# Optimization experiments

Measured on AMD Instinct MI355X. Metric: run time of the kernel, lower is better.

Reference implementation:

```python
import jax, jax.numpy as jnp
import numpy as np

B = 1
T_FRAMES = 512
LDIM = 512
D = 512
H = 8
DH = 64
L = 8
FF = 2048
CTX = 250
RATIOS = (8, 6, 5, 4)
MAX_PERIOD = 10000.0


def setup_inputs() -> dict:
    key = jax.random.key(0)
    ks = iter(jax.random.split(key, 80))
    def rn(shape, s=0.02):
        return jax.random.normal(next(ks), shape, jnp.float32) * s
    inp = {}
    inp['latent'] = rn((B, LDIM, T_FRAMES), 1.0)
    inp['emb_std'] = jax.random.uniform(next(ks), (LDIM,), jnp.float32, 0.5, 1.5)
    inp['emb_mean'] = rn((LDIM,), 0.1)
    inp['quant_w'] = rn((D, LDIM)); inp['quant_b'] = jnp.zeros((D,))
    inp['up_w'] = rn((D, D, 4)); inp['up_b'] = jnp.zeros((D,))
    inp['n1w'] = jnp.ones((L, D)); inp['n1b'] = jnp.zeros((L, D))
    inp['ipw'] = rn((L, 3 * D, D)); inp['ipb'] = jnp.zeros((L, 3 * D))
    inp['opw'] = rn((L, D, D)); inp['opb'] = jnp.zeros((L, D))
    inp['ls1'] = jnp.full((L, D), 0.01)
    inp['n2w'] = jnp.ones((L, D)); inp['n2b'] = jnp.zeros((L, D))
    inp['l1w'] = rn((L, FF, D)); inp['l1b'] = jnp.zeros((L, FF))
    inp['l2w'] = rn((L, D, FF)); inp['l2b'] = jnp.zeros((L, D))
    inp['ls2'] = jnp.full((L, D), 0.01)
    inp['tproj_w'] = rn((D, D)); inp['tproj_b'] = jnp.zeros((D,))
    inp['dc0_w'] = rn((1024, D, 7)); inp['dc0_b'] = jnp.zeros((1024,))
    ch = 1024
    for i, r in enumerate(RATIOS, 1):
        co = ch // 2
        inp['t%d_w' % i] = rn((ch, co, 2 * r)); inp['t%d_b' % i] = jnp.zeros((co,))
        inp['r%da_w' % i] = rn((co // 2, co, 3)); inp['r%da_b' % i] = jnp.zeros((co // 2,))
        inp['r%db_w' % i] = rn((co, co // 2, 1)); inp['r%db_b' % i] = jnp.zeros((co,))
        ch = co
    inp['df_w'] = rn((1, 64, 7)); inp['df_b'] = jnp.zeros((1,))
    return {k: jnp.asarray(v, jnp.float32) for k, v in inp.items()}


def _ln(x, w, b):
    m = x.mean(-1, keepdims=True)
    v = ((x - m) ** 2).mean(-1, keepdims=True)
    return (x - m) / jnp.sqrt(v + 1e-5) * w + b


def _rope(x, cos, sin):
    # x: (B,T,H,DH); cos/sin: (T,1,DH//2)
    b_, t_, h_, d_ = x.shape
    xr = x.reshape(b_, t_, h_, d_ // 2, 2)
    re, im = xr[..., 0], xr[..., 1]
    out = jnp.stack([re * cos - im * sin, re * sin + im * cos], axis=-1)
    return out.reshape(b_, t_, h_, d_)


def _conv(x, w, b, stride=1):
    # StreamingConv1d non-streaming: left-pad by k-stride (zeros), then valid conv.
    k = w.shape[-1]
    pad = k - stride
    if pad > 0:
        x = jnp.pad(x, ((0, 0), (0, 0), (pad, 0)))
    y = jax.lax.conv_general_dilated(x, w, (stride,), 'VALID',
                                     dimension_numbers=('NCH', 'OIH', 'NCH'))
    return y + b[None, :, None]


def _convtr(x, w, b, stride):
    # torch ConvTranspose1d, padding=0: w is (in, out, k); L_out=(L-1)*stride+k
    k = w.shape[-1]
    w2 = jnp.swapaxes(jnp.flip(w, -1), 0, 1)  # (out, in, k)
    y = jax.lax.conv_general_dilated(x, w2, (1,), [(k - 1, k - 1)],
                                     lhs_dilation=(stride,),
                                     dimension_numbers=('NCH', 'OIH', 'NCH'))
    return y + b[None, :, None]


def _forward(latent, emb_std, emb_mean, quant_w, quant_b, up_w, up_b,
             n1w, n1b, ipw, ipb, opw, opb, ls1, n2w, n2b, l1w, l1b, l2w, l2b, ls2,
             tproj_w, tproj_b, dc0_w, dc0_b,
             t1_w, t1_b, r1a_w, r1a_b, r1b_w, r1b_b,
             t2_w, t2_b, r2a_w, r2a_b, r2b_w, r2b_b,
             t3_w, t3_b, r3a_w, r3a_b, r3b_w, r3b_b,
             t4_w, t4_b, r4a_w, r4a_b, r4b_w, r4b_b,
             df_w, df_b):
    # denormalize + quantizer output proj (1x1 conv)
    x = latent * emb_std[None, :, None] + emb_mean[None, :, None]
    x = jnp.einsum('od,bdt->bot', quant_w, x) + quant_b[None, :, None]
    # upsample (raw convtr, no trimming)
    x = _convtr(x, up_w, up_b, 2)
    z = jnp.swapaxes(x, 1, 2)  # (B, T, D)
    T = z.shape[1]
    # windowed causal additive mask: attend to previous `CTX` positions incl. self
    pos = jnp.arange(T)
    delta = pos[:, None] - pos[None, :]
    mask = jnp.where((delta >= 0) & (delta < CTX), 0.0, -jnp.inf).astype(jnp.float32)
    # RoPE tables (offset = 0)
    fr = jnp.exp(jnp.arange(DH // 2, dtype=jnp.float32) * (-np.log(MAX_PERIOD) * 2.0 / DH))
    ang = jnp.arange(T, dtype=jnp.float32)[:, None, None] * fr  # (T,1,DH//2)
    cos, sin = jnp.cos(ang), jnp.sin(ang)
    scale = 1.0 / np.sqrt(DH)

    def step(h, p):
        n1w_, n1b_, ipw_, ipb_, opw_, opb_, ls1_, n2w_, n2b_, l1w_, l1b_, l2w_, l2b_, ls2_ = p
        hn = _ln(h, n1w_, n1b_)
        qkv = (jnp.einsum('btd,ed->bte', hn, ipw_) + ipb_).reshape(B, T, 3, H, DH)
        q, k, v = qkv[:, :, 0], qkv[:, :, 1], qkv[:, :, 2]
        q = _rope(q, cos, sin)
        k = _rope(k, cos, sin)
        s = jnp.einsum('bqhd,bkhd->bhqk', q, k) * scale + mask
        a = jax.nn.softmax(s, axis=-1)
        o = jnp.einsum('bhqk,bkhd->bqhd', a, v).reshape(B, T, D)
        o = jnp.einsum('btd,ed->bte', o, opw_) + opb_
        h = h + ls1_ * o
        hn2 = _ln(h, n2w_, n2b_)
        ff = jax.nn.gelu(jnp.einsum('btd,fd->btf', hn2, l1w_) + l1b_, approximate=False)
        ff = jnp.einsum('btf,df->btd', ff, l2w_) + l2b_
        h = h + ls2_ * ff
        return h, None

    z, _ = jax.lax.scan(step, z, (n1w, n1b, ipw, ipb, opw, opb, ls1,
                                  n2w, n2b, l1w, l1b, l2w, l2b, ls2))
    z = jnp.einsum('btd,ed->bte', z, tproj_w) + tproj_b
    z = jnp.swapaxes(z, 1, 2)  # (B, D, T)
    # SEANet decoder
    z = _conv(z, dc0_w, dc0_b, 1)
    stages = ((t1_w, t1_b, r1a_w, r1a_b, r1b_w, r1b_b, 8),
              (t2_w, t2_b, r2a_w, r2a_b, r2b_w, r2b_b, 6),
              (t3_w, t3_b, r3a_w, r3a_b, r3b_w, r3b_b, 5),
              (t4_w, t4_b, r4a_w, r4a_b, r4b_w, r4b_b, 4))
    for tw, tb, raw_, rab_, rbw_, rbb_, st in stages:
        z = jax.nn.elu(z)
        z = _convtr(z, tw, tb, st)
        v2 = _conv(jax.nn.elu(z), raw_, rab_, 1)
        v2 = _conv(jax.nn.elu(v2), rbw_, rbb_, 1)
        z = z + v2  # residual block skip
    z = jax.nn.elu(z)
    z = _conv(z, df_w, df_b, 1)
    return z  # (B, 1, T_samples)


def reference(latent, emb_std, emb_mean, quant_w, quant_b, up_w, up_b,
              n1w, n1b, ipw, ipb, opw, opb, ls1, n2w, n2b, l1w, l1b, l2w, l2b, ls2,
              tproj_w, tproj_b, dc0_w, dc0_b,
              t1_w, t1_b, r1a_w, r1a_b, r1b_w, r1b_b,
              t2_w, t2_b, r2a_w, r2a_b, r2b_w, r2b_b,
              t3_w, t3_b, r3a_w, r3a_b, r3b_w, r3b_b,
              t4_w, t4_b, r4a_w, r4a_b, r4b_w, r4b_b,
              df_w, df_b):
    return _forward(latent, emb_std, emb_mean, quant_w, quant_b, up_w, up_b,
                    n1w, n1b, ipw, ipb, opw, opb, ls1, n2w, n2b, l1w, l1b, l2w, l2b, ls2,
                    tproj_w, tproj_b, dc0_w, dc0_b,
                    t1_w, t1_b, r1a_w, r1a_b, r1b_w, r1b_b,
                    t2_w, t2_b, r2a_w, r2a_b, r2b_w, r2b_b,
                    t3_w, t3_b, r3a_w, r3a_b, r3b_w, r3b_b,
                    t4_w, t4_b, r4a_w, r4a_b, r4b_w, r4b_b,
                    df_w, df_b)
```

## Files before the change

### kernel.cpp

```cpp
#include <hip/hip_runtime.h>
#include <math.h>

typedef __attribute__((ext_vector_type(8))) short short8;
typedef __attribute__((ext_vector_type(4))) float f32x4;

#define MFMA16(a, b, c) __builtin_amdgcn_mfma_f32_16x16x32_bf16((a), (b), (c), 0, 0, 0)

__device__ __forceinline__ unsigned bfu(float f) {
    unsigned u = __float_as_uint(f);
    return (u + 0x7fffu + ((u >> 16) & 1u)) >> 16;
}

__device__ __forceinline__ void swz_block(unsigned& bx, unsigned& by, unsigned& bz) {
    unsigned gx = gridDim.x, gy = gridDim.y, gz = gridDim.z;
    unsigned nb = gx * gy * gz;
    unsigned d = blockIdx.x + gx * (blockIdx.y + gy * blockIdx.z);
    if ((nb & 7u) == 0u) d = (d & 7u) * (nb >> 3) + (d >> 3);
    bx = d % gx;
    unsigned r = d / gx;
    by = r % gy;
    bz = r / gy;
}

static constexpr int TT   = 1026;
static constexpr int T_S1 = 8216;
static constexpr int T_S2 = 49302;
static constexpr int T_S3 = 246515;
static constexpr int T_S4 = 986064;

static constexpr int NCH    = 8;
static constexpr int LC     = T_S4 / NCH;
static constexpr int LE_MAX = LC + 8;

static constexpr size_t O_X0  = 0;
static constexpr size_t O_XQ  = 262144;
static constexpr size_t O_XU  = 524288;
static constexpr size_t O_Z   = 1049600;
static constexpr size_t O_HN  = 1574912;
static constexpr size_t O_QKV = 2100224;
static constexpr size_t O_AO  = 3676160;
static constexpr size_t O_FF  = 4201472;
static constexpr size_t O_COS = 6302720;
static constexpr size_t O_SIN = 6335552;
static constexpr size_t O_ZT  = 6368384;
static constexpr size_t O_ZC  = 6893696;
static constexpr size_t O_D0  = 7419008;
static constexpr size_t O_Z1  = 8469632;
static constexpr size_t O_V1  = 12676224;
static constexpr size_t O_PS1 = 16000000;
static constexpr size_t O_Z2  = 31553920;
static constexpr size_t O_V2  = 0;
static constexpr size_t O_Z3  = 0;
static constexpr size_t O_V3  = 31553920;
static constexpr size_t O_Z4C = 31553920;
static constexpr size_t O_VAC = 39442944;
static constexpr size_t O_WS4 = 43388928;
static constexpr size_t O_WS3 = 44176256;

static inline int cdiv(int a, int b) { return (a + b - 1) / b; }

__global__ __launch_bounds__(256) void addp_k(float* __restrict__ y,
    const float* __restrict__ p, unsigned long long pstr, int np, int n4)
{
    int i = blockIdx.x * 256 + threadIdx.x;
    if (i >= n4) return;
    float4 s = ((float4*)y)[i];
    for (int z = 0; z < np; z++) {
        float4 q = ((const float4*)(p + (size_t)z * pstr))[i];
        s.x += q.x; s.y += q.y; s.z += q.z; s.w += q.w;
    }
    ((float4*)y)[i] = s;
}

__global__ __launch_bounds__(256) void wreorder_tr(const float* __restrict__ w,
    float* __restrict__ wp, int Ci, int Co, int S, int n)
{
    int i = blockIdx.x * 256 + threadIdx.x;
    if (i >= n) return;
    int o = i / (Ci * 2), r = i - o * (Ci * 2);
    int ci = r >> 1, j = r & 1;
    int co = o / S, p = o - co * S;
    wp[i] = w[((size_t)ci * Co + co) * (2 * S) + (1 - j) * S + p];
}

__global__ __launch_bounds__(256) void embed_k(const float* __restrict__ lat,
    const float* __restrict__ sd, const float* __restrict__ mn, float* __restrict__ y)
{
    int i = blockIdx.x * 256 + threadIdx.x;
    if (i >= 512 * 512) return;
    int c = i >> 9;
    y[i] = lat[i] * sd[c] + mn[c];
}

__global__ __launch_bounds__(256) void rope_tables(float* __restrict__ cs, float* __restrict__ sn)
{
    int idx = blockIdx.x * 256 + threadIdx.x;
    if (idx >= TT * 32) return;
    int i = idx & 31;
    int t = idx >> 5;
    float fr = expf(-(float)i * (logf(10000.f) / 32.f));
    float ang = (float)t * fr;
    cs[idx] = cosf(ang);
    sn[idx] = sinf(ang);
}

__global__ __launch_bounds__(256) void rope_apply(float* __restrict__ qkv,
    const float* __restrict__ cs, const float* __restrict__ sn)
{
    int idx = blockIdx.x * 256 + threadIdx.x;
    if (idx >= TT * 8 * 32) return;
    int i = idx & 31;
    int h = (idx >> 5) & 7;
    int t = idx >> 8;
    float c = cs[t * 32 + i], s = sn[t * 32 + i];
    size_t base = (size_t)t * 1536 + h * 64 + 2 * i;
    float re = qkv[base], im = qkv[base + 1];
    qkv[base]     = re * c - im * s;
    qkv[base + 1] = re * s + im * c;
    base += 512;
    re = qkv[base]; im = qkv[base + 1];
    qkv[base]     = re * c - im * s;
    qkv[base + 1] = re * s + im * c;
}

__global__ __launch_bounds__(256) void transpose_k(const float* __restrict__ in,
    float* __restrict__ out, int R, int C)
{
    __shared__ float tile[32][33];
    int c0 = blockIdx.x * 32, r0 = blockIdx.y * 32;
    int tx = threadIdx.x & 31, ty = threadIdx.x >> 5;
    for (int dy = ty; dy < 32; dy += 8) {
        int r = r0 + dy, c = c0 + tx;
        tile[dy][tx] = (r < R && c < C) ? in[(size_t)r * C + c] : 0.f;
    }
    __syncthreads();
    for (int dy = ty; dy < 32; dy += 8) {
        int c = c0 + dy, r = r0 + tx;
        if (c < C && r < R) out[(size_t)c * R + r] = tile[tx][dy];
    }
}

__global__ __launch_bounds__(256) void ln_kernel(const float* __restrict__ x,
    const float* __restrict__ w, const float* __restrict__ b, float* __restrict__ y)
{
    int t = blockIdx.x, tid = threadIdx.x;
    const float* xr = x + (size_t)t * 512;
    float v0 = xr[tid], v1 = xr[tid + 256];
    float s = v0 + v1, q = v0 * v0 + v1 * v1;
    for (int off = 32; off; off >>= 1) {
        s += __shfl_down(s, off);
        q += __shfl_down(q, off);
    }
    __shared__ float ss[4], qq[4], mb[2];
    int wid = tid >> 6, lane = tid & 63;
    if (lane == 0) { ss[wid] = s; qq[wid] = q; }
    __syncthreads();
    if (tid == 0) {
        float S = ss[0] + ss[1] + ss[2] + ss[3];
        float Q = qq[0] + qq[1] + qq[2] + qq[3];
        float m = S * (1.f / 512.f);
        float var = Q * (1.f / 512.f) - m * m;
        mb[0] = m;
        mb[1] = rsqrtf(var + 1e-5f);
    }
    __syncthreads();
    float m = mb[0], inv = mb[1];
    y[(size_t)t * 512 + tid]       = (v0 - m) * inv * w[tid] + b[tid];
    y[(size_t)t * 512 + tid + 256] = (v1 - m) * inv * w[tid + 256] + b[tid + 256];
}

__global__ __launch_bounds__(256) void attn_kernel(const float* __restrict__ qkv,
    float* __restrict__ o)
{
    int t = blockIdx.x, h = blockIdx.y, tid = threadIdx.x;
    __shared__ float sq[64];
    __shared__ float sp[256];
    __shared__ float red[256];
    __shared__ float pacc[4][64];
    int klo = t - 249; if (klo < 0) klo = 0;
    int kc = t - klo + 1;
    if (tid < 64) sq[tid] = qkv[(size_t)t * 1536 + h * 64 + tid];
    __syncthreads();
    float sval = -3.0e38f;
    if (tid < kc) {
        const float* kr = qkv + (size_t)(klo + tid) * 1536 + 512 + h * 64;
        float d = 0.f;
#pragma unroll 8
        for (int i = 0; i < 64; i++) d += sq[i] * kr[i];
        sval = d * 0.125f;
    }
    red[tid] = sval;
    __syncthreads();
    for (int s2 = 128; s2 > 0; s2 >>= 1) {
        if (tid < s2) red[tid] = fmaxf(red[tid], red[tid + s2]);
        __syncthreads();
    }
    float m = red[0];
    __syncthreads();
    float p = (tid < kc) ? __expf(sval - m) : 0.f;
    sp[tid] = p;
    red[tid] = p;
    __syncthreads();
    for (int s2 = 128; s2 > 0; s2 >>= 1) {
        if (tid < s2) red[tid] += red[tid + s2];
        __syncthreads();
    }
    float inv = 1.f / red[0];
    int d = tid & 63, g = tid >> 6;
    float a = 0.f;
#pragma unroll 4
    for (int kk = g; kk < kc; kk += 4)
        a += sp[kk] * qkv[(size_t)(klo + kk) * 1536 + 1024 + h * 64 + d];
    pacc[g][d] = a;
    __syncthreads();
    if (tid < 64) {
        float r = (pacc[0][tid] + pacc[1][tid] + pacc[2][tid] + pacc[3][tid]) * inv;
        o[(size_t)t * 512 + h * 64 + tid] = r;
    }
}

template <int EPI>
__global__ __launch_bounds__(256, 3) void mfma_gemm(const float* __restrict__ A,
    const float* __restrict__ Wt, const float* __restrict__ bias,
    const float* __restrict__ ls, float* __restrict__ C, int M, int N, int K)
{
    constexpr int STR = 72;
    __shared__ unsigned short sA[128 * STR];
    __shared__ unsigned short sB[128 * STR];
    int tid = threadIdx.x;
    unsigned bxs, bys, bzs; swz_block(bxs, bys, bzs);
    int m0 = bys * 128, n0 = bxs * 128;
    int w = tid >> 6, lane = tid & 63;
    int wm = (w >> 1) * 64, wn = (w & 1) * 64;
    int row15 = lane & 15, q8 = (lane >> 4) * 8;
    int rb = tid >> 3;
    int sg = (tid & 7) * 8;
    f32x4 acc[4][4] = {};
    float4 av[8], bv[8];
    const float4 z4 = make_float4(0.f, 0.f, 0.f, 0.f);

    auto prefetch = [&](int k0) {
#pragma unroll
        for (int it = 0; it < 4; it++) {
            int r = rb + it * 32;
            int gm = m0 + r;
            if (gm < M) {
                const float4* p = (const float4*)(A + (size_t)gm * K + k0 + sg);
                av[2 * it] = p[0]; av[2 * it + 1] = p[1];
            } else { av[2 * it] = z4; av[2 * it + 1] = z4; }
            int gn = n0 + r;
            if (gn < N) {
                const float4* p = (const float4*)(Wt + (size_t)gn * K + k0 + sg);
                bv[2 * it] = p[0]; bv[2 * it + 1] = p[1];
            } else { bv[2 * it] = z4; bv[2 * it + 1] = z4; }
        }
    };

    prefetch(0);
    for (int k0 = 0; k0 < K; k0 += 64) {
        __syncthreads();
#pragma unroll
        for (int it = 0; it < 4; it++) {
            int r = rb + it * 32;
            unsigned* d = (unsigned*)&sA[r * STR + sg];
            float4 f0 = av[2 * it], f1 = av[2 * it + 1];
            d[0] = bfu(f0.x) | (bfu(f0.y) << 16); d[1] = bfu(f0.z) | (bfu(f0.w) << 16);
            d[2] = bfu(f1.x) | (bfu(f1.y) << 16); d[3] = bfu(f1.z) | (bfu(f1.w) << 16);
            d = (unsigned*)&sB[r * STR + sg];
            f0 = bv[2 * it]; f1 = bv[2 * it + 1];
            d[0] = bfu(f0.x) | (bfu(f0.y) << 16); d[1] = bfu(f0.z) | (bfu(f0.w) << 16);
            d[2] = bfu(f1.x) | (bfu(f1.y) << 16); d[3] = bfu(f1.z) | (bfu(f1.w) << 16);
        }
        __syncthreads();
        if (k0 + 64 < K) prefetch(k0 + 64);
#pragma unroll
        for (int kk = 0; kk < 64; kk += 32) {
            short8 af[4], bf[4];
#pragma unroll
            for (int f = 0; f < 4; f++) {
                af[f] = *(const short8*)&sA[(wm + f * 16 + row15) * STR + kk + q8];
                bf[f] = *(const short8*)&sB[(wn + f * 16 + row15) * STR + kk + q8];
            }
#pragma unroll
            for (int i = 0; i < 4; i++)
#pragma unroll
                for (int j = 0; j < 4; j++)
                    acc[i][j] = MFMA16(af[i], bf[j], acc[i][j]);
        }
    }
    int rq = (lane >> 4) * 4;
#pragma unroll
    for (int i = 0; i < 4; i++) {
#pragma unroll
        for (int r = 0; r < 4; r++) {
            int m = m0 + wm + i * 16 + rq + r;
            if (m >= M) continue;
#pragma unroll
            for (int j = 0; j < 4; j++) {
                int n = n0 + wn + j * 16 + row15;
                float v = acc[i][j][r] + bias[n];
                size_t idx = (size_t)m * N + n;
                if (EPI == 0) C[idx] = v;
                else if (EPI == 1) C[idx] = 0.5f * v * (1.f + erff(v * 0.70710678118654752f));
                else C[idx] += ls[n] * v;
            }
        }
    }
}

template <int K, int SHF, bool ELU_IN, bool ACC, bool PART>
__global__ __launch_bounds__(256, 2) void mfma_conv(
    const float* __restrict__ x, const float* __restrict__ w,
    const float* __restrict__ bias, float* __restrict__ y, float* __restrict__ part,
    unsigned long long pstr,
    int Ci, int Co, int x_str, int Tx, int x_t0, int Ty, int y_t0, int to_lo, int to_hi,
    int sh_lo, int sh_hi, int nz)
{
    constexpr int TL = 128 + K - 1;
    constexpr int SX = 40;
    constexpr int SW = 40;
    constexpr int NX = (32 * TL + 255) / 256;
    constexpr int NW4 = 2 * K;
    constexpr int LTS = (SHF > 0) ? 64 * 130 : 1;
    __shared__ unsigned short sX[TL * SX];
    __shared__ unsigned short sW[K * 64 * SW];
    __shared__ float ldsT[LTS];
    int tid = threadIdx.x;
    unsigned bxs, bys, bzs; swz_block(bxs, bys, bzs);
    int co0 = bys * 64;
    int t_base = to_lo + bxs * 128;
    int zi = (int)bzs;
    int cpz = (Ci / 32) / nz;
    int ci_b = zi * cpz * 32, ci_e = ci_b + cpz * 32;
    int w_id = tid >> 6, lane = tid & 63;
    int wm = (w_id >> 1) * 32, wn = (w_id & 1) * 64;
    int row15 = lane & 15, q8 = (lane >> 4) * 8;
    f32x4 acc[2][4] = {};
    float xv[NX];
    float4 wv4[NW4];
    const float4 z4 = make_float4(0.f, 0.f, 0.f, 0.f);

    auto prefetch = [&](int ci0) {
#pragma unroll
        for (int it = 0; it < NX; it++) {
            int i = tid + it * 256;
            float v = 0.f;
            if (i < 32 * TL) {
                int ci = i / TL, tl = i - ci * TL;
                int gl = t_base - (K - 1) + tl - x_t0;
                if (gl >= 0 && gl < Tx) v = x[(size_t)(ci0 + ci) * x_str + gl];
            }
            xv[it] = v;
        }
#pragma unroll
        for (int it = 0; it < NW4; it++) {
            int i4 = tid + it * 256;
            int co = i4 / (8 * K), r4 = i4 - co * (8 * K);
            wv4[it] = (co0 + co < Co)
                ? *(const float4*)(w + ((size_t)(co0 + co) * Ci + ci0) * K + r4 * 4)
                : z4;
        }
    };
    auto commit = [&]() {
#pragma unroll
        for (int it = 0; it < NX; it++) {
            int i = tid + it * 256;
            if (i < 32 * TL) {
                int ci = i / TL, tl = i - ci * TL;
                float v = xv[it];
                if (ELU_IN) v = v > 0.f ? v : __expf(v) - 1.f;
                sX[tl * SX + ci] = (unsigned short)bfu(v);
            }
        }
#pragma unroll
        for (int it = 0; it < NW4; it++) {
            int i4 = tid + it * 256;
            int co = i4 / (8 * K), r4 = i4 - co * (8 * K);
            float4 f = wv4[it];
#pragma unroll
            for (int e = 0; e < 4; e++) {
                int k = r4 * 4 + e;
                int ci = k / K, j = k - ci * K;
                float fv = (e == 0) ? f.x : (e == 1) ? f.y : (e == 2) ? f.z : f.w;
                sW[(j * 64 + co) * SW + ci] = (unsigned short)bfu(fv);
            }
        }
    };

    prefetch(ci_b);
    for (int ci0 = ci_b; ci0 < ci_e; ci0 += 32) {
        __syncthreads();
        commit();
        __syncthreads();
        if (ci0 + 32 < ci_e) prefetch(ci0 + 32);
#pragma unroll
        for (int j = 0; j < K; j++) {
            short8 af[2], bf[4];
#pragma unroll
            for (int f = 0; f < 2; f++)
                af[f] = *(const short8*)&sW[(j * 64 + wm + f * 16 + row15) * SW + q8];
#pragma unroll
            for (int f = 0; f < 4; f++)
                bf[f] = *(const short8*)&sX[(wn + f * 16 + row15 + j) * SX + q8];
#pragma unroll
            for (int i = 0; i < 2; i++)
#pragma unroll
                for (int f = 0; f < 4; f++)
                    acc[i][f] = MFMA16(af[i], bf[f], acc[i][f]);
        }
    }
    int rq = (lane >> 4) * 4;
    if constexpr (SHF > 0) {
        __syncthreads();
#pragma unroll
        for (int i = 0; i < 2; i++) {
#pragma unroll
            for (int r = 0; r < 4; r++) {
                int ol = wm + i * 16 + rq + r;
                float b = bias[(co0 + ol) / SHF];
#pragma unroll
                for (int f = 0; f < 4; f++) {
                    int tl = wn + f * 16 + row15;
                    ldsT[ol * 130 + tl] = acc[i][f][r] + b;
                }
            }
        }
        __syncthreads();
        int co_lo = co0 / SHF;
        int cnt = (co0 + 63) / SHF - co_lo + 1;
        int tot = cnt * 128 * SHF;
        for (int e = tid; e < tot; e += 256) {
            int cr = e / (128 * SHF), u = e - cr * (128 * SHF);
            int t_rel = u / SHF, p = u - t_rel * SHF;
            int co = co_lo + cr;
            int o = co * SHF + p - co0;
            int to = (t_base + t_rel) * SHF + p;
            if (o >= 0 && o < 64 && to >= sh_lo && to < sh_hi)
                y[(size_t)co * Ty + (to - y_t0)] = ldsT[o * 130 + t_rel];
        }
    } else {
#pragma unroll
        for (int i = 0; i < 2; i++) {
#pragma unroll
            for (int r = 0; r < 4; r++) {
                int co = co0 + wm + i * 16 + rq + r;
                if (co >= Co) continue;
                float b = bias[co];
#pragma unroll
                for (int f = 0; f < 4; f++) {
                    int t = t_base + wn + f * 16 + row15;
                    if (t < to_hi) {
                        size_t idx = (size_t)co * Ty + (t - y_t0);
                        if (PART && zi > 0) {
                            part[(size_t)(zi - 1) * pstr + idx] = acc[i][f][r];
                        } else {
                            float v = acc[i][f][r] + b;
                            if (ACC) y[idx] += v; else y[idx] = v;
                        }
                    }
                }
            }
        }
    }
}

__global__ __launch_bounds__(256) void conv7_out_chunk(const float* __restrict__ z4c,
    const float* __restrict__ w, const float* __restrict__ bias,
    float* __restrict__ out, int ext0, int t0, int cnt)
{
    __shared__ float ws_w[64 * 7];
    int tl = blockIdx.x * 256 + threadIdx.x;
    for (int i = threadIdx.x; i < 448; i += 256) ws_w[i] = w[i];
    __syncthreads();
    if (tl >= cnt) return;
    int t = t0 + tl;
    float acc = bias[0];
    for (int ci = 0; ci < 64; ci++) {
        const float* xr = z4c + (size_t)ci * LE_MAX;
#pragma unroll
        for (int j = 0; j < 7; j++) {
            int tg = t - 6 + j;
            float v = 0.f;
            if (tg >= 0) {
                float z = xr[tg - ext0];
                v = z > 0.f ? z : __expf(z) - 1.f;
            }
            acc += ws_w[ci * 7 + j] * v;
        }
    }
    out[t] = acc;
}

template <int K, bool ELU_IN, bool ACC, bool PART>
static void conv_launch(const float* x, const float* w, const float* b, float* y,
    float* part, unsigned long long pstr,
    int Ci, int Co, int x_str, int Tx, int x_t0, int Ty, int y_t0, int to_lo, int to_hi,
    int nz, hipStream_t stream)
{
    dim3 g(cdiv(to_hi - to_lo, 128), cdiv(Co, 64), nz);
    mfma_conv<K, 0, ELU_IN, ACC, PART><<<g, 256, 0, stream>>>(x, w, b, y, part, pstr,
        Ci, Co, x_str, Tx, x_t0, Ty, y_t0, to_lo, to_hi, 0, 0, nz);
}

template <int S, bool ELU_IN>
static void convtr2_launch(const float* x, const float* wp, const float* b, float* y,
    int Ci, int Co, int Ti, int Ty, int y_t0, int to_lo, int to_hi, hipStream_t stream)
{
    int q_lo = to_lo / S;
    int q_hi = cdiv(to_hi, S);
    dim3 g(cdiv(q_hi - q_lo, 128), (Co * S) / 64, 1);
    mfma_conv<2, S, ELU_IN, false, false><<<g, 256, 0, stream>>>(x, wp, b, y, nullptr, 0,
        Ci, Co * S, Ti, Ti, 0, Ty, y_t0, q_lo, q_hi, to_lo, to_hi, 1);
}

extern "C" void kernel_launch(void* const* d_in, const int* in_sizes, int n_in,
                              void* d_out, int out_size, void* d_ws, size_t ws_size,
                              hipStream_t stream)
{
    const float* latent  = (const float*)d_in[0];
    const float* emb_std = (const float*)d_in[1];
    const float* emb_mean= (const float*)d_in[2];
    const float* quant_w = (const float*)d_in[3];
    const float* quant_b = (const float*)d_in[4];
    const float* up_w    = (const float*)d_in[5];
    const float* up_b    = (const float*)d_in[6];
    const float* n1w     = (const float*)d_in[7];
    const float* n1b     = (const float*)d_in[8];
    const float* ipw     = (const float*)d_in[9];
    const float* ipb     = (const float*)d_in[10];
    const float* opw     = (const float*)d_in[11];
    const float* opb     = (const float*)d_in[12];
    const float* ls1     = (const float*)d_in[13];
    const float* n2w     = (const float*)d_in[14];
    const float* n2b     = (const float*)d_in[15];
    const float* l1w     = (const float*)d_in[16];
    const float* l1b     = (const float*)d_in[17];
    const float* l2w     = (const float*)d_in[18];
    const float* l2b     = (const float*)d_in[19];
    const float* ls2     = (const float*)d_in[20];
    const float* tproj_w = (const float*)d_in[21];
    const float* tproj_b = (const float*)d_in[22];
    const float* dc0_w   = (const float*)d_in[23];
    const float* dc0_b   = (const float*)d_in[24];
    const float* df_w    = (const float*)d_in[49];
    const float* df_b    = (const float*)d_in[50];

    float* W = (float*)d_ws;
    float* OUT = (float*)d_out;

    embed_k<<<cdiv(512 * 512, 256), 256, 0, stream>>>(latent, emb_std, emb_mean, W + O_X0);
    conv_launch<1, false, false, true>(W + O_X0, quant_w, quant_b, W + O_XQ,
        W + O_QKV, 262144ULL, 512, 512, 512, 512, 0, 512, 0, 0, 512, 4, stream);
    addp_k<<<cdiv(262144 / 4, 256), 256, 0, stream>>>(W + O_XQ, W + O_QKV, 262144ULL, 3, 262144 / 4);
    wreorder_tr<<<cdiv(1048576, 256), 256, 0, stream>>>(up_w, W + O_QKV, 512, 512, 2, 1048576);
    convtr2_launch<2, false>(W + O_XQ, W + O_QKV, up_b, W + O_XU,
        512, 512, 512, TT, 0, 0, TT, stream);
    transpose_k<<<dim3(cdiv(TT, 32), cdiv(512, 32)), 256, 0, stream>>>(W + O_XU, W + O_Z, 512, TT);
    rope_tables<<<cdiv(TT * 32, 256), 256, 0, stream>>>(W + O_COS, W + O_SIN);

    for (int l = 0; l < 8; l++) {
        ln_kernel<<<TT, 256, 0, stream>>>(W + O_Z, n1w + l * 512, n1b + l * 512, W + O_HN);
        mfma_gemm<0><<<dim3(1536 / 128, cdiv(TT, 128)), 256, 0, stream>>>(
            W + O_HN, ipw + (size_t)l * 1536 * 512, ipb + l * 1536, nullptr, W + O_QKV, TT, 1536, 512);
        rope_apply<<<cdiv(TT * 8 * 32, 256), 256, 0, stream>>>(W + O_QKV, W + O_COS, W + O_SIN);
        attn_kernel<<<dim3(TT, 8), 256, 0, stream>>>(W + O_QKV, W + O_AO);
        mfma_gemm<2><<<dim3(512 / 128, cdiv(TT, 128)), 256, 0, stream>>>(
            W + O_AO, opw + (size_t)l * 512 * 512, opb + l * 512, ls1 + l * 512, W + O_Z, TT, 512, 512);
        ln_kernel<<<TT, 256, 0, stream>>>(W + O_Z, n2w + l * 512, n2b + l * 512, W + O_HN);
        mfma_gemm<1><<<dim3(2048 / 128, cdiv(TT, 128)), 256, 0, stream>>>(
            W + O_HN, l1w + (size_t)l * 2048 * 512, l1b + l * 2048, nullptr, W + O_FF, TT, 2048, 512);
        mfma_gemm<2><<<dim3(512 / 128, cdiv(TT, 128)), 256, 0, stream>>>(
            W + O_FF, l2w + (size_t)l * 512 * 2048, l2b + l * 512, ls2 + l * 512, W + O_Z, TT, 512, 2048);
    }

    mfma_gemm<0><<<dim3(512 / 128, cdiv(TT, 128)), 256, 0, stream>>>(
        W + O_Z, tproj_w, tproj_b, nullptr, W + O_ZT, TT, 512, 512);
    transpose_k<<<dim3(cdiv(512, 32), cdiv(TT, 32)), 256, 0, stream>>>(W + O_ZT, W + O_ZC, TT, 512);
    conv_launch<7, false, false, true>(W + O_ZC, dc0_w, dc0_b, W + O_D0,
        W + O_FF, 1050624ULL, 512, 1024, TT, TT, 0, TT, 0, 0, TT, 2, stream);
    addp_k<<<cdiv(1050624 / 4, 256), 256, 0, stream>>>(W + O_D0, W + O_FF, 1050624ULL, 1, 1050624 / 4);

    {
        const float* tw = (const float*)d_in[25]; const float* tb = (const float*)d_in[26];
        const float* raw = (const float*)d_in[27]; const float* rab = (const float*)d_in[28];
        const float* rbw = (const float*)d_in[29]; const float* rbb = (const float*)d_in[30];
        wreorder_tr<<<cdiv(8388608, 256), 256, 0, stream>>>(tw, W + O_PS1, 1024, 512, 8, 8388608);
        convtr2_launch<8, true>(W + O_D0, W + O_PS1, tb, W + O_Z1,
            1024, 512, TT, T_S1, 0, 0, T_S1, stream);
        conv_launch<3, true, false, true>(W + O_Z1, raw, rab, W + O_V1,
            W + O_PS1, 2103296ULL, 512, 256, T_S1, T_S1, 0, T_S1, 0, 0, T_S1, 2, stream);
        addp_k<<<cdiv(2103296 / 4, 256), 256, 0, stream>>>(W + O_V1, W + O_PS1, 2103296ULL, 1, 2103296 / 4);
        conv_launch<1, true, true, false>(W + O_V1, rbw, rbb, W + O_Z1,
            nullptr, 0ULL, 256, 512, T_S1, T_S1, 0, T_S1, 0, 0, T_S1, 1, stream);
    }
    {
        const float* tw = (const float*)d_in[31]; const float* tb = (const float*)d_in[32];
        const float* raw = (const float*)d_in[33]; const float* rab = (const float*)d_in[34];
        const float* rbw = (const float*)d_in[35]; const float* rbb = (const float*)d_in[36];
        wreorder_tr<<<cdiv(1572864, 256), 256, 0, stream>>>(tw, W + O_PS1, 512, 256, 6, 1572864);
        convtr2_launch<6, true>(W + O_Z1, W + O_PS1, tb, W + O_Z2,
            512, 256, T_S1, T_S2, 0, 0, T_S2, stream);
        conv_launch<3, true, false, false>(W + O_Z2, raw, rab, W + O_V2,
            nullptr, 0ULL, 256, 128, T_S2, T_S2, 0, T_S2, 0, 0, T_S2, 1, stream);
        conv_launch<1, true, true, false>(W + O_V2, rbw, rbb, W + O_Z2,
            nullptr, 0ULL, 128, 256, T_S2, T_S2, 0, T_S2, 0, 0, T_S2, 1, stream);
    }
    {
        const float* tw = (const float*)d_in[37]; const float* tb = (const float*)d_in[38];
        const float* raw = (const float*)d_in[39]; const float* rab = (const float*)d_in[40];
        const float* rbw = (const float*)d_in[41]; const float* rbb = (const float*)d_in[42];
        wreorder_tr<<<cdiv(327680, 256), 256, 0, stream>>>(tw, W + O_WS3, 256, 128, 5, 327680);
        convtr2_launch<5, true>(W + O_Z2, W + O_WS3, tb, W + O_Z3,
            256, 128, T_S2, T_S3, 0, 0, T_S3, stream);
        conv_launch<3, true, false, false>(W + O_Z3, raw, rab, W + O_V3,
            nullptr, 0ULL, 128, 64, T_S3, T_S3, 0, T_S3, 0, 0, T_S3, 1, stream);
        conv_launch<1, true, true, false>(W + O_V3, rbw, rbb, W + O_Z3,
            nullptr, 0ULL, 64, 128, T_S3, T_S3, 0, T_S3, 0, 0, T_S3, 1, stream);
    }
    {
        const float* tw = (const float*)d_in[43]; const float* tb = (const float*)d_in[44];
        const float* raw = (const float*)d_in[45]; const float* rab = (const float*)d_in[46];
        const float* rbw = (const float*)d_in[47]; const float* rbb = (const float*)d_in[48];
        wreorder_tr<<<cdiv(65536, 256), 256, 0, stream>>>(tw, W + O_WS4, 128, 64, 4, 65536);
        for (int c = 0; c < NCH; c++) {
            int t0 = c * LC;
            int ext0 = (c == 0) ? 0 : t0 - 8;
            int Le = t0 + LC - ext0;
            int vlo = (c == 0) ? 0 : ext0 + 2;
            convtr2_launch<4, true>(W + O_Z3, W + O_WS4, tb, W + O_Z4C,
                128, 64, T_S3, LE_MAX, ext0, ext0, ext0 + Le, stream);
            conv_launch<3, true, false, false>(W + O_Z4C, raw, rab, W + O_VAC,
                nullptr, 0ULL, 64, 32, LE_MAX, Le, ext0, LE_MAX, ext0, vlo, ext0 + Le, 1, stream);
            conv_launch<1, true, true, false>(W + O_VAC, rbw, rbb, W + O_Z4C,
                nullptr, 0ULL, 32, 64, LE_MAX, Le, ext0, LE_MAX, ext0, vlo, ext0 + Le, 1, stream);
            conv7_out_chunk<<<dim3(cdiv(LC, 256), 1), 256, 0, stream>>>(
                W + O_Z4C, df_w, df_b, OUT, ext0, t0, LC);
        }
    }
}
```

Baseline: 6.560 ms.

## Alias conv epilogue LDS onto staging buffers, raise occupancy, reorder block swizzle

The transpose buffer used by the shuffle epilogue now shares storage with the X/W staging buffers, and the epilogue writes out in two 64-column halves so it fits inside that smaller region. The kernel's launch bounds request 4 blocks per SM instead of 2, and a new swizzle walks the output-channel dimension fastest so neighbouring blocks reuse the same input time tile. The goal is more resident blocks per CU and better cache locality on the input. In exchange the epilogue gains an extra pair of barriers, and the tighter register budget could cause spills.

```diff
diff --git a/kernel.cpp b/kernel.cpp
--- a/kernel.cpp
+++ b/kernel.cpp
@@ -20,6 +20,17 @@
     unsigned r = d / gx;
     by = r % gy;
     bz = r / gy;
+}
+
+__device__ __forceinline__ void swz_conv(unsigned& bx, unsigned& by, unsigned& bz) {
+    unsigned gx = gridDim.x, gy = gridDim.y, gz = gridDim.z;
+    unsigned nb = gx * gy * gz;
+    unsigned d = blockIdx.x + gx * (blockIdx.y + gy * blockIdx.z);
+    if ((nb & 7u) == 0u) d = (d & 7u) * (nb >> 3) + (d >> 3);
+    by = d % gy;
+    unsigned r = d / gy;
+    bx = r % gx;
+    bz = r / gx;
 }
 
 static constexpr int TT   = 1026;
@@ -309,7 +320,7 @@
 }
 
 template <int K, int SHF, bool ELU_IN, bool ACC, bool PART>
-__global__ __launch_bounds__(256, 2) void mfma_conv(
+__global__ __launch_bounds__(256, 4) void mfma_conv(
     const float* __restrict__ x, const float* __restrict__ w,
     const float* __restrict__ bias, float* __restrict__ y, float* __restrict__ part,
     unsigned long long pstr,
@@ -321,12 +332,15 @@
     constexpr int SW = 40;
     constexpr int NX = (32 * TL + 255) / 256;
     constexpr int NW4 = 2 * K;
-    constexpr int LTS = (SHF > 0) ? 64 * 130 : 1;
-    __shared__ unsigned short sX[TL * SX];
-    __shared__ unsigned short sW[K * 64 * SW];
-    __shared__ float ldsT[LTS];
+    constexpr int SXB = TL * SX;
+    constexpr int SWB = K * 64 * SW;
+    static_assert(SHF == 0 || (SXB + SWB) * 2 >= 64 * 66 * 4, "ldsT alias too big");
+    __shared__ __align__(16) unsigned short shm[SXB + SWB];
+    unsigned short* sX = shm;
+    unsigned short* sW = shm + SXB;
+    float* ldsT = (float*)shm;
     int tid = threadIdx.x;
-    unsigned bxs, bys, bzs; swz_block(bxs, bys, bzs);
+    unsigned bxs, bys, bzs; swz_conv(bxs, bys, bzs);
     int co0 = bys * 64;
     int t_base = to_lo + bxs * 128;
     int zi = (int)bzs;
@@ -411,32 +425,35 @@
     }
     int rq = (lane >> 4) * 4;
     if constexpr (SHF > 0) {
-        __syncthreads();
-#pragma unroll
-        for (int i = 0; i < 2; i++) {
-#pragma unroll
-            for (int r = 0; r < 4; r++) {
-                int ol = wm + i * 16 + rq + r;
-                float b = bias[(co0 + ol) / SHF];
-#pragma unroll
-                for (int f = 0; f < 4; f++) {
-                    int tl = wn + f * 16 + row15;
-                    ldsT[ol * 130 + tl] = acc[i][f][r] + b;
-                }
-            }
-        }
-        __syncthreads();
         int co_lo = co0 / SHF;
         int cnt = (co0 + 63) / SHF - co_lo + 1;
-        int tot = cnt * 128 * SHF;
-        for (int e = tid; e < tot; e += 256) {
-            int cr = e / (128 * SHF), u = e - cr * (128 * SHF);
-            int t_rel = u / SHF, p = u - t_rel * SHF;
-            int co = co_lo + cr;
-            int o = co * SHF + p - co0;
-            int to = (t_base + t_rel) * SHF + p;
-            if (o >= 0 && o < 64 && to >= sh_lo && to < sh_hi)
-                y[(size_t)co * Ty + (to - y_t0)] = ldsT[o * 130 + t_rel];
+        int tot = cnt * 64 * SHF;
+#pragma unroll
+        for (int h = 0; h < 2; h++) {
+            __syncthreads();
+            if (wn == h * 64) {
+#pragma unroll
+                for (int i = 0; i < 2; i++) {
+#pragma unroll
+                    for (int r = 0; r < 4; r++) {
+                        int ol = wm + i * 16 + rq + r;
+                        float b = bias[(co0 + ol) / SHF];
+#pragma unroll
+                        for (int f = 0; f < 4; f++)
+                            ldsT[ol * 66 + f * 16 + row15] = acc[i][f][r] + b;
+                    }
+                }
+            }
+            __syncthreads();
+            for (int e = tid; e < tot; e += 256) {
+                int cr = e / (64 * SHF), u = e - cr * (64 * SHF);
+                int tr = u / SHF, p = u - tr * SHF;
+                int co = co_lo + cr;
+                int o = co * SHF + p - co0;
+                int to = (t_base + h * 64 + tr) * SHF + p;
+                if (o >= 0 && o < 64 && to >= sh_lo && to < sh_hi)
+                    y[(size_t)co * Ty + (to - y_t0)] = ldsT[o * 66 + tr];
+            }
         }
     } else {
 #pragma unroll
```

After: 7.511 ms. 1.14x slower.
